# Kernel tuning notes

Measured on AMD Instinct MI355X. Metric: run time of the kernel, lower is better.

The kernel has to match this reference:

```python
import jax, jax.numpy as jnp
import numpy as np

B, N, EPG, D, V = 512, 100, 1600, 128, 20215
K1, K2 = 80, 64  # ceil(0.8*100), ceil(0.8*80)


def setup_inputs() -> dict:
    key = jax.random.key(0)
    ks = jax.random.split(key, 14)
    x_idx = jax.random.randint(ks[0], (B * N,), 0, V)
    off = (jnp.arange(B) * N)[:, None]
    src = (jax.random.randint(ks[1], (B, EPG), 0, N) + off).reshape(-1)
    dst = (jax.random.randint(ks[2], (B, EPG), 0, N) + off).reshape(-1)
    edge_index = jnp.stack([src, dst])
    batch = jnp.repeat(jnp.arange(B), N)
    s = 1.0 / np.sqrt(D)
    return {
        "x_idx": x_idx,
        "edge_index": edge_index,
        "batch": batch,
        "emb": jax.random.normal(ks[3], (V, D), jnp.float32),
        "Wl": jax.random.normal(ks[4], (D, D), jnp.float32) * s,
        "bl": jnp.zeros((D,), jnp.float32),
        "Wr": jax.random.normal(ks[5], (D, D), jnp.float32) * s,
        "pw1": jax.random.normal(ks[6], (D,), jnp.float32) * s,
        "pw2": jax.random.normal(ks[7], (D,), jnp.float32) * s,
        "W1": jax.random.normal(ks[8], (2 * D, 64), jnp.float32) * (1.0 / np.sqrt(2 * D)),
        "b1": jnp.zeros((64,), jnp.float32),
        "W3": jax.random.normal(ks[9], (64, 1), jnp.float32) * 0.125,
        "b3": jnp.zeros((1,), jnp.float32),
    }


def _topk_pool(h, w, k):
    # h: [B, n, D]; PyG TopKPooling: score = tanh((h @ w)/||w||), keep top-k, scale by score
    score = jnp.tanh(jnp.einsum("bnd,d->bn", h, w) / jnp.linalg.norm(w))
    vals, idx = jax.lax.top_k(score, k)  # [B, k]
    hp = jnp.take_along_axis(h, idx[..., None], axis=1) * vals[..., None]
    return hp


def _readout(hp):
    # global max pool || global mean pool -> [B, 2D]
    return jnp.concatenate([hp.max(axis=1), hp.mean(axis=1)], axis=-1)


def reference(x_idx, edge_index, batch, emb, Wl, bl, Wr, pw1, pw2, W1, b1, W3, b3):
    Nt = x_idx.shape[0]
    h = emb[x_idx]  # [Nt, D]
    src, dst = edge_index[0], edge_index[1]
    # SAGEConv: mean-aggregate source features at destinations
    agg = jax.ops.segment_sum(h[src], dst, num_segments=Nt)
    deg = jax.ops.segment_sum(jnp.ones((src.shape[0],), h.dtype), dst, num_segments=Nt)
    mean = agg / jnp.maximum(deg, 1.0)[:, None]
    h = jax.nn.relu(mean @ Wl + bl + h @ Wr)

    hg = h.reshape(B, N, D)
    hp1 = _topk_pool(hg, pw1, K1)   # [B, K1, D]
    x1 = _readout(hp1)              # [B, 2D]
    hp2 = _topk_pool(hp1, pw2, K2)  # [B, K2, D]
    x2 = _readout(hp2)

    x = x1 + x2
    x = jax.nn.relu(x @ W1 + b1)
    # dropout is identity in eval mode
    out = jax.nn.sigmoid(x @ W3 + b3).squeeze(-1)  # [B]
    return out
```

## Files before the change

kernel.cpp:

```cpp
#include <hip/hip_runtime.h>
#include <hip/hip_bf16.h>
#include <math.h>

#define BGRAPH 512
#define NNODE  100
#define EPG    1600
#define DIM    128
#define ETOT   (BGRAPH * EPG)
#define PAD    132
#define K1     80
#define K2     64
#define NTHREADS 1024

typedef __attribute__((ext_vector_type(8))) short short8;
typedef __attribute__((ext_vector_type(4))) short short4v;
typedef __attribute__((ext_vector_type(4))) float f32x4;

__device__ __forceinline__ ushort bf16_rne(float x) {
    unsigned u = __float_as_uint(x);
    u += 0x7FFFu + ((u >> 16) & 1u);
    return (ushort)(u >> 16);
}
__device__ __forceinline__ float bf16f(ushort h) {
    return __uint_as_float(((unsigned)h) << 16);
}

__global__ __launch_bounds__(256) void wprep(const float* __restrict__ Wl,
                                             const float* __restrict__ Wr,
                                             ushort* __restrict__ whi,
                                             ushort* __restrict__ wlo) {
    int t = blockIdx.x * 256 + threadIdx.x;
    if (t >= 8 * 8 * 64) return;
    int lane = t & 63, ks = (t >> 6) & 7, nt = t >> 9;
    int n  = nt * 16 + (lane & 15);
    int kb = ks * 32 + 8 * (lane >> 4);
#pragma unroll
    for (int j = 0; j < 8; ++j) {
        int k = kb + j;
        float w = (k < 128) ? Wl[k * 128 + n] : Wr[(k - 128) * 128 + n];
        ushort hi = bf16_rne(w);
        whi[t * 8 + j] = hi;
        wlo[t * 8 + j] = bf16_rne(w - bf16f(hi));
    }
}


__global__ __launch_bounds__(NTHREADS) void fused_gnn(
    const int*   __restrict__ x_idx,
    const int*   __restrict__ edge_index,
    const float* __restrict__ emb,
    const float* __restrict__ blv,
    const float* __restrict__ pw1,
    const float* __restrict__ pw2,
    const float* __restrict__ W1,
    const float* __restrict__ b1g,
    const float* __restrict__ W3,
    const float* __restrict__ b3g,
    const ushort* __restrict__ whi,
    const ushort* __restrict__ wlo,
    float*       __restrict__ out)
{
    __shared__ __align__(16) float Xf[128 * PAD];
    __shared__ __align__(16) int   Zi[128 * PAD];
    __shared__ int degi[NNODE];
    __shared__ int nid[NNODE];
    __shared__ float score1[NNODE], q2[NNODE], s2v[NNODE];
    __shared__ int   rank1[NNODE], rank2[NNODE];
    __shared__ float xv[2 * DIM];

    const int g    = blockIdx.x;
    const int tid  = threadIdx.x;
    const int lane = tid & 63;
    const int wv   = tid >> 6;
    const int mg = wv >> 2, ng = wv & 3;

    {
        int4* z4 = reinterpret_cast<int4*>(Zi);
        for (int i = tid; i < 128 * PAD / 4; i += NTHREADS) z4[i] = int4{0, 0, 0, 0};
        float4* xz = reinterpret_cast<float4*>(Xf + 100 * PAD);
        for (int i = tid; i < 28 * PAD / 4; i += NTHREADS) xz[i] = float4{0, 0, 0, 0};
        if (tid < NNODE) { nid[tid] = x_idx[g * NNODE + tid]; degi[tid] = 0; }
    }
    __syncthreads();

    {
        const float4* emb4 = reinterpret_cast<const float4*>(emb);
        for (int i = tid; i < NNODE * 32; i += NTHREADS) {
            int n = i >> 5, q = i & 31;
            float4 v = emb4[nid[n] * 32 + q];
            *reinterpret_cast<float4*>(&Xf[n * PAD + q * 4]) = v;
        }
        for (int i = tid; i < EPG; i += NTHREADS) {
            int s = edge_index[g * EPG + i] - g * NNODE;
            int d = edge_index[ETOT + g * EPG + i] - g * NNODE;
            atomicAdd(&Zi[d * PAD + s], 1);
            atomicAdd(&degi[d], 1);
        }
    }
    __syncthreads();

    ushort* ahhi = reinterpret_cast<ushort*>(Xf);
    ushort* ahlo = ahhi + 16384;
    ushort* abf  = reinterpret_cast<ushort*>(Zi);

    {
        const int m  = tid >> 3;
        const int kb = (tid & 7) * 16;
        float hv[16];
        int   cv[16];
#pragma unroll
        for (int u = 0; u < 4; ++u) {
            float4 v = *reinterpret_cast<const float4*>(&Xf[m * PAD + kb + 4 * u]);
            hv[4 * u] = v.x; hv[4 * u + 1] = v.y; hv[4 * u + 2] = v.z; hv[4 * u + 3] = v.w;
            int4 c = *reinterpret_cast<const int4*>(&Zi[m * PAD + kb + 4 * u]);
            cv[4 * u] = c.x; cv[4 * u + 1] = c.y; cv[4 * u + 2] = c.z; cv[4 * u + 3] = c.w;
        }
        __syncthreads();
#pragma unroll
        for (int g2 = 0; g2 < 2; ++g2) {
            int idx = ((m >> 4) * 4 + (kb >> 5)) * 512 +
                      ((m & 15) + 16 * (((kb >> 3) + g2) & 3)) * 8;
            short8 hh, hl, ab;
#pragma unroll
            for (int j = 0; j < 8; ++j) {
                float v = hv[g2 * 8 + j];
                ushort hb = bf16_rne(v);
                hh[j] = (short)hb;
                hl[j] = (short)bf16_rne(v - bf16f(hb));
                ab[j] = (short)bf16_rne((float)cv[g2 * 8 + j]);
            }
            *reinterpret_cast<short8*>(&ahhi[idx]) = hh;
            *reinterpret_cast<short8*>(&ahlo[idx]) = hl;
            *reinterpret_cast<short8*>(&abf[idx])  = ab;
        }
    }
    __syncthreads();

    f32x4 accP[2][2], accQ[2][2];
#pragma unroll
    for (int im = 0; im < 2; ++im)
#pragma unroll
        for (int in = 0; in < 2; ++in) {
            accP[im][in] = f32x4{0.f, 0.f, 0.f, 0.f};
            accQ[im][in] = f32x4{0.f, 0.f, 0.f, 0.f};
        }
#pragma unroll
    for (int ks = 0; ks < 4; ++ks) {
        short8 Ah[2], Al[2];
#pragma unroll
        for (int im = 0; im < 2; ++im) {
            int fi = (((2 * mg + im) * 4 + ks) * 64 + lane) * 8;
            Ah[im] = *reinterpret_cast<const short8*>(&ahhi[fi]);
            Al[im] = *reinterpret_cast<const short8*>(&ahlo[fi]);
        }
        short8 BhL[2], BlL[2], BhR[2], BlR[2];
#pragma unroll
        for (int in = 0; in < 2; ++in) {
            int nt = 2 * ng + in;
            int tL = ((nt * 8 + ks) * 64 + lane) * 8;
            int tR = ((nt * 8 + ks + 4) * 64 + lane) * 8;
            BhL[in] = *reinterpret_cast<const short8*>(whi + tL);
            BlL[in] = *reinterpret_cast<const short8*>(wlo + tL);
            BhR[in] = *reinterpret_cast<const short8*>(whi + tR);
            BlR[in] = *reinterpret_cast<const short8*>(wlo + tR);
        }
#pragma unroll
        for (int im = 0; im < 2; ++im)
#pragma unroll
            for (int in = 0; in < 2; ++in) {
                accP[im][in] = __builtin_amdgcn_mfma_f32_16x16x32_bf16(Ah[im], BhL[in], accP[im][in], 0, 0, 0);
                accP[im][in] = __builtin_amdgcn_mfma_f32_16x16x32_bf16(Al[im], BhL[in], accP[im][in], 0, 0, 0);
                accP[im][in] = __builtin_amdgcn_mfma_f32_16x16x32_bf16(Ah[im], BlL[in], accP[im][in], 0, 0, 0);
                accQ[im][in] = __builtin_amdgcn_mfma_f32_16x16x32_bf16(Ah[im], BhR[in], accQ[im][in], 0, 0, 0);
                accQ[im][in] = __builtin_amdgcn_mfma_f32_16x16x32_bf16(Al[im], BhR[in], accQ[im][in], 0, 0, 0);
                accQ[im][in] = __builtin_amdgcn_mfma_f32_16x16x32_bf16(Ah[im], BlR[in], accQ[im][in], 0, 0, 0);
            }
    }
    __syncthreads();

    {
        ushort* pbhi = ahhi;
        ushort* pblo = ahlo;
#pragma unroll
        for (int im = 0; im < 2; ++im) {
            int row0 = (2 * mg + im) * 16 + 4 * (lane >> 4);
#pragma unroll
            for (int in = 0; in < 2; ++in) {
                int col = (2 * ng + in) * 16 + (lane & 15);
                int idx = ((col >> 4) * 4 + (row0 >> 5)) * 512 +
                          ((col & 15) + 16 * ((row0 >> 3) & 3)) * 8 + (row0 & 7);
                short4v h4, l4;
#pragma unroll
                for (int r = 0; r < 4; ++r) {
                    float v = accP[im][in][r];
                    ushort hb = bf16_rne(v);
                    h4[r] = (short)hb;
                    l4[r] = (short)bf16_rne(v - bf16f(hb));
                }
                *reinterpret_cast<short4v*>(&pbhi[idx]) = h4;
                *reinterpret_cast<short4v*>(&pblo[idx]) = l4;
            }
        }
    }
    __syncthreads();

    f32x4 accR[2][2];
#pragma unroll
    for (int im = 0; im < 2; ++im)
#pragma unroll
        for (int in = 0; in < 2; ++in) accR[im][in] = f32x4{0.f, 0.f, 0.f, 0.f};
#pragma unroll
    for (int ks = 0; ks < 4; ++ks) {
        short8 Ab[2];
#pragma unroll
        for (int im = 0; im < 2; ++im)
            Ab[im] = *reinterpret_cast<const short8*>(&abf[(((2 * mg + im) * 4 + ks) * 64 + lane) * 8]);
        short8 Bh[2], Bl[2];
#pragma unroll
        for (int in = 0; in < 2; ++in) {
            int fi = (((2 * ng + in) * 4 + ks) * 64 + lane) * 8;
            Bh[in] = *reinterpret_cast<const short8*>(&ahhi[fi]);
            Bl[in] = *reinterpret_cast<const short8*>(&ahlo[fi]);
        }
#pragma unroll
        for (int im = 0; im < 2; ++im)
#pragma unroll
            for (int in = 0; in < 2; ++in) {
                accR[im][in] = __builtin_amdgcn_mfma_f32_16x16x32_bf16(Ab[im], Bh[in], accR[im][in], 0, 0, 0);
                accR[im][in] = __builtin_amdgcn_mfma_f32_16x16x32_bf16(Ab[im], Bl[in], accR[im][in], 0, 0, 0);
            }
    }
    __syncthreads();

#pragma unroll
    for (int im = 0; im < 2; ++im) {
        int rbase = (2 * mg + im) * 16 + 4 * (lane >> 4);
#pragma unroll
        for (int in = 0; in < 2; ++in) {
            int col = (2 * ng + in) * 16 + (lane & 15);
            float bc = blv[col];
#pragma unroll
            for (int r = 0; r < 4; ++r) {
                int row = rbase + r;
                if (row < NNODE) {
                    float invd = 1.0f / fmaxf((float)degi[row], 1.0f);
                    Xf[row * PAD + col] = fmaxf(accR[im][in][r] * invd + accQ[im][in][r] + bc, 0.0f);
                }
            }
        }
    }
    __syncthreads();

    {
        float a1 = pw1[lane], c1 = pw1[lane + 64];
        float a2 = pw2[lane], c2 = pw2[lane + 64];
        float n1 = a1 * a1 + c1 * c1;
        float n2 = a2 * a2 + c2 * c2;
#pragma unroll
        for (int off = 32; off; off >>= 1) {
            n1 += __shfl_xor(n1, off);
            n2 += __shfl_xor(n2, off);
        }
        float rn1 = 1.0f / sqrtf(n1);
        float rn2 = 1.0f / sqrtf(n2);

        for (int n = wv; n < NNODE; n += 16) {
            float hA = Xf[n * PAD + lane], hB = Xf[n * PAD + lane + 64];
            float d1 = hA * a1 + hB * c1;
            float d2 = hA * a2 + hB * c2;
#pragma unroll
            for (int off = 32; off; off >>= 1) {
                d1 += __shfl_xor(d1, off);
                d2 += __shfl_xor(d2, off);
            }
            if (lane == 0) {
                score1[n] = tanhf(d1 * rn1);
                q2[n]     = d2 * rn2;
            }
        }
    }
    __syncthreads();

    if (tid < NNODE) {
        float si = score1[tid];
        int r = 0;
        for (int j = 0; j < NNODE; ++j) {
            float sj = score1[j];
            r += (sj > si || (sj == si && j < tid)) ? 1 : 0;
        }
        rank1[tid] = r;
        s2v[tid] = tanhf(score1[tid] * q2[tid]);
    }
    __syncthreads();

    if (tid < NNODE) {
        int r1i = rank1[tid];
        if (r1i < K1) {
            float si = s2v[tid];
            int r = 0;
            for (int j = 0; j < NNODE; ++j) {
                if (rank1[j] < K1) {
                    float sj = s2v[j];
                    r += (sj > si || (sj == si && rank1[j] < r1i)) ? 1 : 0;
                }
            }
            rank2[tid] = r;
        } else {
            rank2[tid] = 1 << 30;
        }
    }
    __syncthreads();

    {
        float* Zf = reinterpret_cast<float*>(Zi);
        float* redm1 = Zf;
        float* reds1 = Zf + 1024;
        float* redm2 = Zf + 2048;
        float* reds2 = Zf + 3072;
        int f = tid & 127;
        int c = tid >> 7;
        float mx1 = -INFINITY, sm1 = 0.0f, mx2 = -INFINITY, sm2 = 0.0f;
        for (int n = c; n < NNODE; n += 8) {
            if (rank1[n] < K1) {
                float v1 = Xf[n * PAD + f] * score1[n];
                mx1 = fmaxf(mx1, v1);
                sm1 += v1;
                if (rank2[n] < K2) {
                    float v2 = v1 * s2v[n];
                    mx2 = fmaxf(mx2, v2);
                    sm2 += v2;
                }
            }
        }
        redm1[c * DIM + f] = mx1; reds1[c * DIM + f] = sm1;
        redm2[c * DIM + f] = mx2; reds2[c * DIM + f] = sm2;
        __syncthreads();
        if (tid < DIM) {
            float m1 = -INFINITY, s1 = 0.0f, m2 = -INFINITY, s2 = 0.0f;
#pragma unroll
            for (int cc = 0; cc < 8; ++cc) {
                m1 = fmaxf(m1, redm1[cc * DIM + tid]); s1 += reds1[cc * DIM + tid];
                m2 = fmaxf(m2, redm2[cc * DIM + tid]); s2 += reds2[cc * DIM + tid];
            }
            xv[tid]       = m1 + m2;
            xv[DIM + tid] = s1 * (1.0f / K1) + s2 * (1.0f / K2);
        }
    }
    __syncthreads();

    {
        float* Zf = reinterpret_cast<float*>(Zi);
        float* part = Zf + 4096;
        int o = tid & 63, ch = tid >> 6;
        float acc = 0.0f;
#pragma unroll
        for (int u = 0; u < 16; ++u) {
            int f = ch * 16 + u;
            acc += xv[f] * W1[f * 64 + o];
        }
        part[ch * 64 + o] = acc;
        __syncthreads();
        if (tid < 64) {
            float a2 = b1g[tid];
#pragma unroll
            for (int cc = 0; cc < 16; ++cc) a2 += part[cc * 64 + tid];
            float y = fmaxf(a2, 0.0f);
            float r = y * W3[tid];
#pragma unroll
            for (int off = 32; off; off >>= 1) r += __shfl_xor(r, off);
            if (tid == 0) out[g] = 1.0f / (1.0f + expf(-(r + b3g[0])));
        }
    }
}

extern "C" void kernel_launch(void* const* d_in, const int* in_sizes, int n_in,
                              void* d_out, int out_size, void* d_ws, size_t ws_size,
                              hipStream_t stream) {
    const int*   x_idx      = (const int*)d_in[0];
    const int*   edge_index = (const int*)d_in[1];
    const float* emb = (const float*)d_in[3];
    const float* Wl  = (const float*)d_in[4];
    const float* bl  = (const float*)d_in[5];
    const float* Wr  = (const float*)d_in[6];
    const float* pw1 = (const float*)d_in[7];
    const float* pw2 = (const float*)d_in[8];
    const float* W1  = (const float*)d_in[9];
    const float* b1  = (const float*)d_in[10];
    const float* W3  = (const float*)d_in[11];
    const float* b3  = (const float*)d_in[12];
    float* out = (float*)d_out;

    ushort* whi = (ushort*)d_ws;
    ushort* wlo = (ushort*)((char*)d_ws + 65536);

    wprep<<<16, 256, 0, stream>>>(Wl, Wr, whi, wlo);
    fused_gnn<<<BGRAPH, NTHREADS, 0, stream>>>(
        x_idx, edge_index, emb, bl, pw1, pw2, W1, b1, W3, b3, whi, wlo, out);
}
```

Measured before the change: 153.9 us.

## Split fused GNN kernel into gather, MFMA and pooling kernels via workspace

Replaces the single 1024-thread fused kernel, which uses a large shared-memory footprint, with three kernels. The first gathers embeddings and builds the packed bf16 adjacency and inverse degrees. The second runs the split-bf16 MFMA GEMMs at 512 threads with far less LDS. The third does top-k pooling and the MLP head. All intermediates go through global workspace. The goal is higher occupancy and less per-block serialisation, at the cost of extra global round trips, extra launches, and a dependence on a large enough workspace; it falls back to the fused kernel otherwise.

```diff
diff --git a/kernel.cpp b/kernel.cpp
--- a/kernel.cpp
+++ b/kernel.cpp
@@ -10,7 +10,12 @@
 #define PAD    132
 #define K1     80
 #define K2     64
-#define NTHREADS 1024
+
+#define OFF_W    0ULL
+#define OFF_AHL  131072ULL
+#define OFF_AB   (131072ULL + 33554432ULL)
+#define OFF_INV  (OFF_AB + 16777216ULL)
+#define WS_NEED  (OFF_INV + 262144ULL)
 
 typedef __attribute__((ext_vector_type(8))) short short8;
 typedef __attribute__((ext_vector_type(4))) short short4v;
@@ -44,8 +49,320 @@
     }
 }
 
-
-__global__ __launch_bounds__(NTHREADS) void fused_gnn(
+__global__ __launch_bounds__(512) void k1_gather(const int* __restrict__ x_idx,
+                                                 const int* __restrict__ edge_index,
+                                                 const float* __restrict__ emb,
+                                                 char* __restrict__ ws)
+{
+    __shared__ int acntW[128 * 64];
+    __shared__ int degi[128];
+    __shared__ int nid[NNODE];
+    const int g = blockIdx.x, tid = threadIdx.x;
+
+    for (int i = tid; i < 128 * 64; i += 512) acntW[i] = 0;
+    if (tid < 128) degi[tid] = 0;
+    if (tid < NNODE) nid[tid] = x_idx[g * NNODE + tid];
+    __syncthreads();
+
+    for (int i = tid; i < EPG; i += 512) {
+        int s = edge_index[g * EPG + i] - g * NNODE;
+        int d = edge_index[ETOT + g * EPG + i] - g * NNODE;
+        atomicAdd(&acntW[d * 64 + (s >> 1)], 1 << (16 * (s & 1)));
+        atomicAdd(&degi[d], 1);
+    }
+
+    ushort* hhi = (ushort*)(ws + OFF_AHL + (size_t)g * 65536);
+    ushort* hlo = hhi + 16384;
+    const float4* emb4 = (const float4*)emb;
+    for (int i = tid; i < NNODE * 16; i += 512) {
+        int n = i >> 4, p = i & 15;
+        float4 a = emb4[nid[n] * 32 + 2 * p];
+        float4 b = emb4[nid[n] * 32 + 2 * p + 1];
+        float vf[8] = {a.x, a.y, a.z, a.w, b.x, b.y, b.z, b.w};
+        short8 hh, hl;
+#pragma unroll
+        for (int j = 0; j < 8; ++j) {
+            ushort hb = bf16_rne(vf[j]);
+            hh[j] = (short)hb;
+            hl[j] = (short)bf16_rne(vf[j] - bf16f(hb));
+        }
+        *reinterpret_cast<short8*>(&hhi[n * 128 + 8 * p]) = hh;
+        *reinterpret_cast<short8*>(&hlo[n * 128 + 8 * p]) = hl;
+    }
+    for (int i = tid; i < 28 * 16; i += 512) {
+        int n = 100 + (i >> 4), p = i & 15;
+        *reinterpret_cast<uint4*>(&hhi[n * 128 + 8 * p]) = uint4{0, 0, 0, 0};
+        *reinterpret_cast<uint4*>(&hlo[n * 128 + 8 * p]) = uint4{0, 0, 0, 0};
+    }
+    __syncthreads();
+
+    ushort* abf = (ushort*)(ws + OFF_AB + (size_t)g * 32768);
+    for (int i = tid; i < 128 * 64; i += 512) {
+        int w = acntW[i];
+        ushort c0 = bf16_rne((float)(w & 0xFFFF));
+        ushort c1 = bf16_rne((float)(((unsigned)w) >> 16));
+        ((unsigned*)abf)[i] = (unsigned)c0 | ((unsigned)c1 << 16);
+    }
+    float* invd = (float*)(ws + OFF_INV + (size_t)g * 512);
+    if (tid < 128) invd[tid] = 1.0f / fmaxf((float)degi[tid], 1.0f);
+}
+
+__global__ __launch_bounds__(512, 4) void k2_mfma(const float* __restrict__ blv,
+                                                  char* __restrict__ ws)
+{
+    __shared__ ushort pbhi[16384];
+    __shared__ ushort pblo[16384];
+    const int g = blockIdx.x, tid = threadIdx.x;
+    const int lane = tid & 63, wv = tid >> 6;
+    const int mgrp = wv >> 1, ngrp = wv & 1;
+
+    const ushort* hhi = (const ushort*)(ws + OFF_AHL + (size_t)g * 65536);
+    const ushort* hlo = hhi + 16384;
+    const ushort* whi = (const ushort*)ws;
+    const ushort* wlo = whi + 32768;
+    const ushort* abf = (const ushort*)(ws + OFF_AB + (size_t)g * 32768);
+    const float*  invd = (const float*)(ws + OFF_INV + (size_t)g * 512);
+
+    f32x4 accP[2][4], accQ[2][4];
+#pragma unroll
+    for (int im = 0; im < 2; ++im)
+#pragma unroll
+        for (int in = 0; in < 4; ++in) {
+            accP[im][in] = f32x4{0.f, 0.f, 0.f, 0.f};
+            accQ[im][in] = f32x4{0.f, 0.f, 0.f, 0.f};
+        }
+
+#pragma unroll
+    for (int ks = 0; ks < 4; ++ks) {
+        const int kb = ks * 32 + 8 * (lane >> 4);
+        short8 Ah[2], Al[2];
+#pragma unroll
+        for (int im = 0; im < 2; ++im) {
+            int m = (2 * mgrp + im) * 16 + (lane & 15);
+            Ah[im] = *reinterpret_cast<const short8*>(&hhi[m * 128 + kb]);
+            Al[im] = *reinterpret_cast<const short8*>(&hlo[m * 128 + kb]);
+        }
+#pragma unroll
+        for (int in = 0; in < 4; ++in) {
+            int nt = 4 * ngrp + in;
+            int tL = ((nt * 8 + ks) * 64 + lane) * 8;
+            int tR = ((nt * 8 + ks + 4) * 64 + lane) * 8;
+            short8 BhL = *reinterpret_cast<const short8*>(whi + tL);
+            short8 BlL = *reinterpret_cast<const short8*>(wlo + tL);
+            short8 BhR = *reinterpret_cast<const short8*>(whi + tR);
+            short8 BlR = *reinterpret_cast<const short8*>(wlo + tR);
+#pragma unroll
+            for (int im = 0; im < 2; ++im) {
+                accP[im][in] = __builtin_amdgcn_mfma_f32_16x16x32_bf16(Ah[im], BhL, accP[im][in], 0, 0, 0);
+                accP[im][in] = __builtin_amdgcn_mfma_f32_16x16x32_bf16(Al[im], BhL, accP[im][in], 0, 0, 0);
+                accP[im][in] = __builtin_amdgcn_mfma_f32_16x16x32_bf16(Ah[im], BlL, accP[im][in], 0, 0, 0);
+                accQ[im][in] = __builtin_amdgcn_mfma_f32_16x16x32_bf16(Ah[im], BhR, accQ[im][in], 0, 0, 0);
+                accQ[im][in] = __builtin_amdgcn_mfma_f32_16x16x32_bf16(Al[im], BhR, accQ[im][in], 0, 0, 0);
+                accQ[im][in] = __builtin_amdgcn_mfma_f32_16x16x32_bf16(Ah[im], BlR, accQ[im][in], 0, 0, 0);
+            }
+        }
+    }
+
+#pragma unroll
+    for (int im = 0; im < 2; ++im) {
+        int row0 = (2 * mgrp + im) * 16 + 4 * (lane >> 4);
+#pragma unroll
+        for (int in = 0; in < 4; ++in) {
+            int col = (4 * ngrp + in) * 16 + (lane & 15);
+            int idx = ((col >> 4) * 4 + (row0 >> 5)) * 512 +
+                      ((col & 15) + 16 * ((row0 >> 3) & 3)) * 8 + (row0 & 7);
+            short4v h4, l4;
+#pragma unroll
+            for (int r = 0; r < 4; ++r) {
+                float v = accP[im][in][r];
+                ushort hb = bf16_rne(v);
+                h4[r] = (short)hb;
+                l4[r] = (short)bf16_rne(v - bf16f(hb));
+            }
+            *reinterpret_cast<short4v*>(&pbhi[idx]) = h4;
+            *reinterpret_cast<short4v*>(&pblo[idx]) = l4;
+        }
+    }
+    __syncthreads();
+
+    f32x4 accR[2][4];
+#pragma unroll
+    for (int im = 0; im < 2; ++im)
+#pragma unroll
+        for (int in = 0; in < 4; ++in) accR[im][in] = f32x4{0.f, 0.f, 0.f, 0.f};
+
+#pragma unroll
+    for (int ks = 0; ks < 4; ++ks) {
+        const int kb = ks * 32 + 8 * (lane >> 4);
+        short8 Ab[2];
+#pragma unroll
+        for (int im = 0; im < 2; ++im) {
+            int m = (2 * mgrp + im) * 16 + (lane & 15);
+            Ab[im] = *reinterpret_cast<const short8*>(&abf[m * 128 + kb]);
+        }
+#pragma unroll
+        for (int in = 0; in < 4; ++in) {
+            int fi = (((4 * ngrp + in) * 4 + ks) * 64 + lane) * 8;
+            short8 Bh = *reinterpret_cast<const short8*>(&pbhi[fi]);
+            short8 Bl = *reinterpret_cast<const short8*>(&pblo[fi]);
+#pragma unroll
+            for (int im = 0; im < 2; ++im) {
+                accR[im][in] = __builtin_amdgcn_mfma_f32_16x16x32_bf16(Ab[im], Bh, accR[im][in], 0, 0, 0);
+                accR[im][in] = __builtin_amdgcn_mfma_f32_16x16x32_bf16(Ab[im], Bl, accR[im][in], 0, 0, 0);
+            }
+        }
+    }
+
+    float* hnew = (float*)(ws + OFF_AHL + (size_t)g * 65536);
+#pragma unroll
+    for (int im = 0; im < 2; ++im) {
+        int rbase = (2 * mgrp + im) * 16 + 4 * (lane >> 4);
+#pragma unroll
+        for (int r = 0; r < 4; ++r) {
+            int row = rbase + r;
+            if (row < NNODE) {
+                float iv = invd[row];
+#pragma unroll
+                for (int in = 0; in < 4; ++in) {
+                    int col = (4 * ngrp + in) * 16 + (lane & 15);
+                    float v = fmaxf(accR[im][in][r] * iv + accQ[im][in][r] + blv[col], 0.0f);
+                    hnew[row * 128 + col] = v;
+                }
+            }
+        }
+    }
+}
+
+__global__ __launch_bounds__(256) void k3_pool(const float* __restrict__ pw1,
+                                               const float* __restrict__ pw2,
+                                               const float* __restrict__ W1,
+                                               const float* __restrict__ b1g,
+                                               const float* __restrict__ W3,
+                                               const float* __restrict__ b3g,
+                                               const char* __restrict__ ws,
+                                               float* __restrict__ out)
+{
+    __shared__ float score1[NNODE], q2s[NNODE], s2v[NNODE];
+    __shared__ int   rank1[NNODE], rank2[NNODE];
+    __shared__ float redm1[2][DIM], reds1[2][DIM], redm2[2][DIM], reds2[2][DIM];
+    __shared__ float xv[2 * DIM];
+    __shared__ float part[4][64];
+
+    const int g = blockIdx.x, tid = threadIdx.x;
+    const int lane = tid & 63, wv = tid >> 6;
+    const float* hnew = (const float*)(ws + OFF_AHL + (size_t)g * 65536);
+
+    {
+        float a1 = pw1[lane], c1 = pw1[lane + 64];
+        float a2 = pw2[lane], c2 = pw2[lane + 64];
+        float n1 = a1 * a1 + c1 * c1;
+        float n2 = a2 * a2 + c2 * c2;
+#pragma unroll
+        for (int off = 32; off; off >>= 1) {
+            n1 += __shfl_xor(n1, off);
+            n2 += __shfl_xor(n2, off);
+        }
+        float rn1 = 1.0f / sqrtf(n1);
+        float rn2 = 1.0f / sqrtf(n2);
+        for (int n = wv; n < NNODE; n += 4) {
+            float hA = hnew[n * 128 + lane], hB = hnew[n * 128 + lane + 64];
+            float d1 = hA * a1 + hB * c1;
+            float d2 = hA * a2 + hB * c2;
+#pragma unroll
+            for (int off = 32; off; off >>= 1) {
+                d1 += __shfl_xor(d1, off);
+                d2 += __shfl_xor(d2, off);
+            }
+            if (lane == 0) {
+                score1[n] = tanhf(d1 * rn1);
+                q2s[n]    = d2 * rn2;
+            }
+        }
+    }
+    __syncthreads();
+
+    if (tid < NNODE) {
+        float si = score1[tid];
+        int r = 0;
+        for (int j = 0; j < NNODE; ++j) {
+            float sj = score1[j];
+            r += (sj > si || (sj == si && j < tid)) ? 1 : 0;
+        }
+        rank1[tid] = r;
+        s2v[tid] = tanhf(score1[tid] * q2s[tid]);
+    }
+    __syncthreads();
+
+    if (tid < NNODE) {
+        int r1i = rank1[tid];
+        if (r1i < K1) {
+            float si = s2v[tid];
+            int r = 0;
+            for (int j = 0; j < NNODE; ++j) {
+                if (rank1[j] < K1) {
+                    float sj = s2v[j];
+                    r += (sj > si || (sj == si && rank1[j] < r1i)) ? 1 : 0;
+                }
+            }
+            rank2[tid] = r;
+        } else {
+            rank2[tid] = 1 << 30;
+        }
+    }
+    __syncthreads();
+
+    {
+        int f = tid & 127;
+        int c = tid >> 7;
+        float mx1 = -INFINITY, sm1 = 0.0f, mx2 = -INFINITY, sm2 = 0.0f;
+        for (int n = c; n < NNODE; n += 2) {
+            if (rank1[n] < K1) {
+                float v1 = hnew[n * 128 + f] * score1[n];
+                mx1 = fmaxf(mx1, v1);
+                sm1 += v1;
+                if (rank2[n] < K2) {
+                    float v2 = v1 * s2v[n];
+                    mx2 = fmaxf(mx2, v2);
+                    sm2 += v2;
+                }
+            }
+        }
+        redm1[c][f] = mx1; reds1[c][f] = sm1;
+        redm2[c][f] = mx2; reds2[c][f] = sm2;
+    }
+    __syncthreads();
+    if (tid < DIM) {
+        float m1 = fmaxf(redm1[0][tid], redm1[1][tid]);
+        float s1 = reds1[0][tid] + reds1[1][tid];
+        float m2 = fmaxf(redm2[0][tid], redm2[1][tid]);
+        float s2 = reds2[0][tid] + reds2[1][tid];
+        xv[tid]       = m1 + m2;
+        xv[DIM + tid] = s1 * (1.0f / K1) + s2 * (1.0f / K2);
+    }
+    __syncthreads();
+
+    {
+        int o = tid & 63, ch = tid >> 6;
+        float acc = 0.0f;
+#pragma unroll 8
+        for (int u = 0; u < 64; ++u) {
+            int fi = ch * 64 + u;
+            acc += xv[fi] * W1[fi * 64 + o];
+        }
+        part[ch][o] = acc;
+        __syncthreads();
+        if (tid < 64) {
+            float a2 = b1g[tid] + part[0][tid] + part[1][tid] + part[2][tid] + part[3][tid];
+            float y = fmaxf(a2, 0.0f);
+            float r = y * W3[tid];
+#pragma unroll
+            for (int off = 32; off; off >>= 1) r += __shfl_xor(r, off);
+            if (tid == 0) out[g] = 1.0f / (1.0f + expf(-(r + b3g[0])));
+        }
+    }
+}
+
+__global__ __launch_bounds__(1024) void fused_gnn(
     const int*   __restrict__ x_idx,
     const int*   __restrict__ edge_index,
     const float* __restrict__ emb,
@@ -76,21 +393,20 @@
 
     {
         int4* z4 = reinterpret_cast<int4*>(Zi);
-        for (int i = tid; i < 128 * PAD / 4; i += NTHREADS) z4[i] = int4{0, 0, 0, 0};
+        for (int i = tid; i < 128 * PAD / 4; i += 1024) z4[i] = int4{0, 0, 0, 0};
         float4* xz = reinterpret_cast<float4*>(Xf + 100 * PAD);
-        for (int i = tid; i < 28 * PAD / 4; i += NTHREADS) xz[i] = float4{0, 0, 0, 0};
+        for (int i = tid; i < 28 * PAD / 4; i += 1024) xz[i] = float4{0, 0, 0, 0};
         if (tid < NNODE) { nid[tid] = x_idx[g * NNODE + tid]; degi[tid] = 0; }
     }
     __syncthreads();
-
     {
         const float4* emb4 = reinterpret_cast<const float4*>(emb);
-        for (int i = tid; i < NNODE * 32; i += NTHREADS) {
+        for (int i = tid; i < NNODE * 32; i += 1024) {
             int n = i >> 5, q = i & 31;
             float4 v = emb4[nid[n] * 32 + q];
             *reinterpret_cast<float4*>(&Xf[n * PAD + q * 4]) = v;
         }
-        for (int i = tid; i < EPG; i += NTHREADS) {
+        for (int i = tid; i < EPG; i += 1024) {
             int s = edge_index[g * EPG + i] - g * NNODE;
             int d = edge_index[ETOT + g * EPG + i] - g * NNODE;
             atomicAdd(&Zi[d * PAD + s], 1);
@@ -177,7 +493,6 @@
             }
     }
     __syncthreads();
-
     {
         ushort* pbhi = ahhi;
         ushort* pblo = ahlo;
@@ -231,7 +546,6 @@
             }
     }
     __syncthreads();
-
 #pragma unroll
     for (int im = 0; im < 2; ++im) {
         int rbase = (2 * mg + im) * 16 + 4 * (lane >> 4);
@@ -250,7 +564,6 @@
         }
     }
     __syncthreads();
-
     {
         float a1 = pw1[lane], c1 = pw1[lane + 64];
         float a2 = pw2[lane], c2 = pw2[lane + 64];
@@ -263,7 +576,6 @@
         }
         float rn1 = 1.0f / sqrtf(n1);
         float rn2 = 1.0f / sqrtf(n2);
-
         for (int n = wv; n < NNODE; n += 16) {
             float hA = Xf[n * PAD + lane], hB = Xf[n * PAD + lane + 64];
             float d1 = hA * a1 + hB * c1;
@@ -280,7 +592,6 @@
         }
     }
     __syncthreads();
-
     if (tid < NNODE) {
         float si = score1[tid];
         int r = 0;
@@ -292,7 +603,6 @@
         s2v[tid] = tanhf(score1[tid] * q2[tid]);
     }
     __syncthreads();
-
     if (tid < NNODE) {
         int r1i = rank1[tid];
         if (r1i < K1) {
@@ -310,7 +620,6 @@
         }
     }
     __syncthreads();
-
     {
         float* Zf = reinterpret_cast<float*>(Zi);
         float* redm1 = Zf;
@@ -347,7 +656,6 @@
         }
     }
     __syncthreads();
-
     {
         float* Zf = reinterpret_cast<float*>(Zi);
         float* part = Zf + 4096;
@@ -394,6 +702,13 @@
     ushort* wlo = (ushort*)((char*)d_ws + 65536);
 
     wprep<<<16, 256, 0, stream>>>(Wl, Wr, whi, wlo);
-    fused_gnn<<<BGRAPH, NTHREADS, 0, stream>>>(
-        x_idx, edge_index, emb, bl, pw1, pw2, W1, b1, W3, b3, whi, wlo, out);
+
+    if (ws_size >= (size_t)WS_NEED) {
+        k1_gather<<<BGRAPH, 512, 0, stream>>>(x_idx, edge_index, emb, (char*)d_ws);
+        k2_mfma<<<BGRAPH, 512, 0, stream>>>(bl, (char*)d_ws);
+        k3_pool<<<BGRAPH, 256, 0, stream>>>(pw1, pw2, W1, b1, W3, b3, (const char*)d_ws, out);
+    } else {
+        fused_gnn<<<BGRAPH, 1024, 0, stream>>>(
+            x_idx, edge_index, emb, bl, pw1, pw2, W1, b1, W3, b3, whi, wlo, out);
+    }
 }
```

Result: slower. 161.3 us (+4.8%).
